# Optimization experiments

Measured on AMD Instinct MI355X. Metric: run time of the kernel, lower is better.

Reference implementation:

```python
import jax, jax.numpy as jnp
import numpy as np
import math

B, T, D = 1, 2048, 2048
H, HD = 16, 128          # n_head, head_dim = D // H
L = 512                  # latent_dims
RD = 64                  # rope_dims
K = 32                   # top-k selected tokens per query
THETA = 10000.0


def rope_tables(rd, t_max):
    freqs = 1.0 / (THETA ** (jnp.arange(0, rd, 2, dtype=jnp.float32) / rd))
    t = jnp.arange(t_max, dtype=jnp.float32)
    ang = jnp.outer(t, freqs)                      # (T, rd/2)
    cos = jnp.concatenate([jnp.cos(ang), jnp.cos(ang)], axis=-1)  # (T, rd)
    sin = jnp.concatenate([jnp.sin(ang), jnp.sin(ang)], axis=-1)
    return cos, sin


def rotate_half(x):
    d = x.shape[-1] // 2
    return jnp.concatenate([-x[..., d:], x[..., :d]], axis=-1)


def apply_rope(x, cos, sin):
    # x: (B, H, T, rd); cos/sin: (T, rd) -> broadcast over B, H
    t = x.shape[2]
    return x * cos[None, None, :t] + rotate_half(x) * sin[None, None, :t]


def setup_inputs() -> dict:
    key = jax.random.key(0)
    ks = jax.random.split(key, 10)
    s = lambda fan_in: 1.0 / math.sqrt(fan_in)
    inp = {
        'x': jax.random.normal(ks[0], (B, T, D), dtype=jnp.float32),
        'Wqd': jax.random.normal(ks[1], (D, L), dtype=jnp.float32) * s(D),
        'Wqu': jax.random.normal(ks[2], (L, D), dtype=jnp.float32) * s(L),
        'Wqr': jax.random.normal(ks[3], (L, H * RD), dtype=jnp.float32) * s(L),
        'Wkvd': jax.random.normal(ks[4], (D, L), dtype=jnp.float32) * s(D),
        'Wku': jax.random.normal(ks[5], (L, D), dtype=jnp.float32) * s(L),
        'Wvu': jax.random.normal(ks[6], (L, D), dtype=jnp.float32) * s(L),
        'Wkr': jax.random.normal(ks[7], (D, RD), dtype=jnp.float32) * s(D),
        'Wo': jax.random.normal(ks[8], (D, D), dtype=jnp.float32) * s(D),
        'topk_idx': jax.random.randint(ks[9], (B, T, K), 0, T, dtype=jnp.int64)
            if jax.config.jax_enable_x64 else
            jax.random.randint(ks[9], (B, T, K), 0, T, dtype=jnp.int32),
    }
    return inp


def reference(x, Wqd, Wqu, Wqr, Wkvd, Wku, Wvu, Wkr, Wo, topk_idx):
    cos, sin = rope_tables(RD, T)

    ql = x @ Wqd                                               # (B,T,L)
    q = (ql @ Wqu).reshape(B, T, H, HD).transpose(0, 2, 1, 3)  # (B,H,T,hd)
    qr = (ql @ Wqr).reshape(B, T, H, RD).transpose(0, 2, 1, 3)
    qr = apply_rope(qr, cos, sin)                              # (B,H,T,rd)

    ckv = x @ Wkvd                                             # (B,T,L)
    k = (ckv @ Wku).reshape(B, T, H, HD).transpose(0, 2, 1, 3) # (B,H,T,hd)
    v = (ckv @ Wvu).reshape(B, T, H, HD).transpose(0, 2, 1, 3)
    kr = apply_rope((x @ Wkr)[:, None], cos, sin)[:, 0]        # (B,T,rd) shared across heads

    # top-k gather sparse attention path
    flat = topk_idx.reshape(B, T * K)                          # (B, T*K)
    k_sel = jax.vmap(lambda a, i: a[:, i])(k, flat).reshape(B, H, T, K, HD)
    v_sel = jax.vmap(lambda a, i: a[:, i])(v, flat).reshape(B, H, T, K, HD)
    kr_sel = jax.vmap(lambda a, i: a[i])(kr, flat).reshape(B, T, K, RD)

    scale = 1.0 / math.sqrt(HD + RD)
    scores = (jnp.einsum('bhtd,bhtkd->bhtk', q, k_sel)
              + jnp.einsum('bhtd,btkd->bhtk', qr, kr_sel)) * scale
    attn = jax.nn.softmax(scores, axis=-1)                     # (B,H,T,K)
    out = jnp.einsum('bhtk,bhtkd->bhtd', attn, v_sel)          # (B,H,T,hd)
    out = out.transpose(0, 2, 1, 3).reshape(B, T, D)
    return out @ Wo
```

## Files before the change

### kernel.cpp

```cpp
#include <hip/hip_runtime.h>
#include <hip/hip_bf16.h>
#include <math.h>

typedef __hip_bfloat16 bf16;
typedef __attribute__((ext_vector_type(4))) float f32x4;
typedef __attribute__((ext_vector_type(8))) short s16x8;

#define T_SEQ 2048
#define DIM   2048
#define NH    16
#define LAT   512
#define RD    64
#define TOPK  32

typedef const __attribute__((address_space(1))) void* gas_ptr;
typedef __attribute__((address_space(3))) void* las_ptr;

struct GGroup {
    const bf16* A; const bf16* BT; bf16* C;
    int K, lda, ldb, ldc;
    int tx, ty, nz;
    long aZ, bZ, cZ;
    int tiles;
    int flags, N, t0;
};
struct GPack { GGroup g[4]; int n; };

template<int MT, int DB>
__global__ __launch_bounds__(256)
void gemm_group(GPack gp)
{
    constexpr int MI = MT / 64;

    int b = blockIdx.x;
    int gi = 0;
    while (gi < gp.n - 1 && b >= gp.g[gi].tiles) { b -= gp.g[gi].tiles; ++gi; }
    const GGroup g = gp.g[gi];

    {
        const int nwg = g.tiles;
        const int xcd = b & 7, idx = b >> 3;
        const int qq = nwg >> 3, rr = nwg & 7;
        b = (xcd < rr ? xcd * (qq + 1) : rr * (qq + 1) + (xcd - rr) * qq) + idx;
    }

    const int per_z = g.tx * g.ty;
    const int z   = b / per_z;
    const int rem = b - z * per_z;
    const int bx  = rem % g.tx;
    const int by  = rem / g.tx;

    const bf16* A  = g.A  + (size_t)z * g.aZ;
    const bf16* BT = g.BT + (size_t)z * g.bZ;
    bf16*       C  = g.C  + (size_t)z * g.cZ;

    __shared__ bf16 aL[(DB + 1) * MT * 64];
    __shared__ bf16 bL[(DB + 1) * 64 * 64];

    const int tid  = threadIdx.x;
    const int wave = tid >> 6;
    const int lane = tid & 63;
    const int quad = lane >> 4;
    const int l16  = lane & 15;

    const int tile_m = by * MT;
    const int tile_n = bx * 64;
    const int wrow = wave * (MT / 4);

    const int lrow = lane >> 3;
    const int lke  = (((lane & 7) ^ lrow) * 8);
    const int sw   = l16 & 7;

    f32x4 acc[MI][4] = {};

    const int nt = g.K >> 6;

    auto stage = [&](int t, int sb) {
        const int k0 = t << 6;
#pragma unroll
        for (int p = 0; p < 2 * MI; ++p) {
            const int R = (wave * 2 * MI + p) * 8;
            const bf16* src = A + (size_t)(tile_m + R + lrow) * g.lda + k0 + lke;
            __builtin_amdgcn_global_load_lds((gas_ptr)src,
                (las_ptr)(aL + sb * MT * 64 + R * 64), 16, 0, 0);
        }
#pragma unroll
        for (int p = 0; p < 2; ++p) {
            const int R = (wave * 2 + p) * 8;
            int brow = tile_n + R + lrow;
            if (g.flags & 2) brow = brow < g.N ? brow : g.N - 1;
            const bf16* src = BT + (size_t)brow * g.ldb + k0 + lke;
            __builtin_amdgcn_global_load_lds((gas_ptr)src,
                (las_ptr)(bL + sb * 4096 + R * 64), 16, 0, 0);
        }
    };

    auto compute = [&](int sb) {
#pragma unroll
        for (int ks = 0; ks < 2; ++ks) {
            s16x8 af[MI], bfr[4];
#pragma unroll
            for (int i = 0; i < MI; ++i)
                af[i] = *(const s16x8*)(&aL[sb * MT * 64 + (wrow + i * 16 + l16) * 64 +
                                            (((ks * 4 + quad) ^ sw) * 8)]);
#pragma unroll
            for (int j = 0; j < 4; ++j)
                bfr[j] = *(const s16x8*)(&bL[sb * 4096 + (j * 16 + l16) * 64 +
                                             (((ks * 4 + quad) ^ sw) * 8)]);

#pragma unroll
            for (int i = 0; i < MI; ++i)
#pragma unroll
                for (int j = 0; j < 4; ++j)
                    acc[i][j] = __builtin_amdgcn_mfma_f32_16x16x32_bf16(
                        af[i], bfr[j], acc[i][j], 0, 0, 0);
        }
    };

    if (DB) {
        stage(0, 0);
        asm volatile("s_waitcnt vmcnt(0)" ::: "memory");
        __builtin_amdgcn_s_barrier();
        int cur = 0;
        for (int t = 0; t < nt; ++t) {
            if (t + 1 < nt) stage(t + 1, cur ^ 1);
            compute(cur);
            asm volatile("s_waitcnt vmcnt(0)" ::: "memory");
            __builtin_amdgcn_s_barrier();
            cur ^= 1;
        }
    } else {
        for (int t = 0; t < nt; ++t) {
            stage(t, 0);
            __syncthreads();
            compute(0);
            __syncthreads();
        }
    }

    if (g.flags & 1) {
#pragma unroll
        for (int jp = 0; jp < 2; ++jp) {
            const int colL = tile_n + jp * 16 + l16;
            if ((g.flags & 2) && colL >= g.N) continue;
            const float fr = powf(10000.f, -(float)(jp * 16 + l16) / 32.f);
#pragma unroll
            for (int i = 0; i < MI; ++i) {
#pragma unroll
                for (int r = 0; r < 4; ++r) {
                    const int row = tile_m + wrow + i * 16 + quad * 4 + r;
                    float sv, cv;
                    sincosf((float)(g.t0 + row) * fr, &sv, &cv);
                    const float x0 = acc[i][jp][r];
                    const float x1 = acc[i][jp + 2][r];
                    C[(size_t)row * g.ldc + colL]      = __float2bfloat16(x0 * cv - x1 * sv);
                    C[(size_t)row * g.ldc + colL + 32] = __float2bfloat16(x1 * cv + x0 * sv);
                }
            }
        }
    } else if (g.flags & 4) {
        float* Cf = (float*)C;
#pragma unroll
        for (int j = 0; j < 4; ++j) {
            const int col = tile_n + j * 16 + l16;
#pragma unroll
            for (int i = 0; i < MI; ++i)
#pragma unroll
                for (int r = 0; r < 4; ++r) {
                    const int row = tile_m + wrow + i * 16 + quad * 4 + r;
                    Cf[(size_t)row * g.ldc + col] = acc[i][j][r];
                }
        }
    } else {
#pragma unroll
        for (int j = 0; j < 4; ++j) {
            const int col = tile_n + j * 16 + l16;
            if ((g.flags & 2) && col >= g.N) continue;
#pragma unroll
            for (int i = 0; i < MI; ++i)
#pragma unroll
                for (int r = 0; r < 4; ++r) {
                    const int row = tile_m + wrow + i * 16 + quad * 4 + r;
                    C[(size_t)row * g.ldc + col] = __float2bfloat16(acc[i][j][r]);
                }
        }
    }
}

template<int DB>
__global__ __launch_bounds__(256)
void gemm128(GPack gp)
{
    int b = blockIdx.x;
    int gi = 0;
    while (gi < gp.n - 1 && b >= gp.g[gi].tiles) { b -= gp.g[gi].tiles; ++gi; }
    const GGroup g = gp.g[gi];

    {
        const int nwg = g.tiles;
        const int xcd = b & 7, idx = b >> 3;
        const int qq = nwg >> 3, rr = nwg & 7;
        b = (xcd < rr ? xcd * (qq + 1) : rr * (qq + 1) + (xcd - rr) * qq) + idx;
    }

    const int per_z = g.tx * g.ty;
    const int z   = b / per_z;
    const int rem = b - z * per_z;
    const int bx  = rem % g.tx;
    const int by  = rem / g.tx;

    const bf16* A  = g.A  + (size_t)z * g.aZ;
    const bf16* BT = g.BT + (size_t)z * g.bZ;
    bf16*       C  = g.C  + (size_t)z * g.cZ;

    __shared__ bf16 aL[(DB + 1) * 128 * 64];
    __shared__ bf16 bL[(DB + 1) * 128 * 64];

    const int tid  = threadIdx.x;
    const int wave = tid >> 6;
    const int lane = tid & 63;
    const int quad = lane >> 4;
    const int l16  = lane & 15;

    const int tile_m = by * 128;
    const int tile_n = bx * 128;
    const int wm = (wave >> 1) * 64;
    const int wn = (wave & 1) * 64;

    const int lrow = lane >> 3;
    const int lke  = (((lane & 7) ^ lrow) * 8);
    const int sw   = l16 & 7;

    f32x4 acc[4][4] = {};

    const int nt = g.K >> 6;

    auto stage = [&](int t, int sb) {
        const int k0 = t << 6;
#pragma unroll
        for (int p = 0; p < 4; ++p) {
            const int R = (wave * 4 + p) * 8;
            const bf16* srcA = A + (size_t)(tile_m + R + lrow) * g.lda + k0 + lke;
            __builtin_amdgcn_global_load_lds((gas_ptr)srcA,
                (las_ptr)(aL + sb * 8192 + R * 64), 16, 0, 0);
            int brow = tile_n + R + lrow;
            if (g.flags & 2) brow = brow < g.N ? brow : g.N - 1;
            const bf16* srcB = BT + (size_t)brow * g.ldb + k0 + lke;
            __builtin_amdgcn_global_load_lds((gas_ptr)srcB,
                (las_ptr)(bL + sb * 8192 + R * 64), 16, 0, 0);
        }
    };

    auto compute = [&](int sb) {
#pragma unroll
        for (int ks = 0; ks < 2; ++ks) {
            const int seg = ((ks * 4 + quad) ^ sw) * 8;
            s16x8 af[4], bf_[4];
#pragma unroll
            for (int i = 0; i < 4; ++i)
                af[i] = *(const s16x8*)(&aL[sb * 8192 + (wm + i * 16 + l16) * 64 + seg]);
#pragma unroll
            for (int j = 0; j < 4; ++j)
                bf_[j] = *(const s16x8*)(&bL[sb * 8192 + (wn + j * 16 + l16) * 64 + seg]);

#pragma unroll
            for (int i = 0; i < 4; ++i)
#pragma unroll
                for (int j = 0; j < 4; ++j)
                    acc[i][j] = __builtin_amdgcn_mfma_f32_16x16x32_bf16(
                        af[i], bf_[j], acc[i][j], 0, 0, 0);
        }
    };

    if (DB) {
        stage(0, 0);
        asm volatile("s_waitcnt vmcnt(0)" ::: "memory");
        __builtin_amdgcn_s_barrier();
        int cur = 0;
        for (int t = 0; t < nt; ++t) {
            if (t + 1 < nt) stage(t + 1, cur ^ 1);
            compute(cur);
            asm volatile("s_waitcnt vmcnt(0)" ::: "memory");
            __builtin_amdgcn_s_barrier();
            cur ^= 1;
        }
    } else {
        for (int t = 0; t < nt; ++t) {
            stage(t, 0);
            __syncthreads();
            compute(0);
            __syncthreads();
        }
    }

    if (g.flags & 1) {
#pragma unroll
        for (int jp = 0; jp < 2; ++jp) {
            const int colL = tile_n + wn + jp * 16 + l16;
            if ((g.flags & 2) && colL >= g.N) continue;
            const float fr = powf(10000.f, -(float)(jp * 16 + l16) / 32.f);
#pragma unroll
            for (int i = 0; i < 4; ++i) {
#pragma unroll
                for (int r = 0; r < 4; ++r) {
                    const int row = tile_m + wm + i * 16 + quad * 4 + r;
                    float sv, cv;
                    sincosf((float)(g.t0 + row) * fr, &sv, &cv);
                    const float x0 = acc[i][jp][r];
                    const float x1 = acc[i][jp + 2][r];
                    C[(size_t)row * g.ldc + colL]      = __float2bfloat16(x0 * cv - x1 * sv);
                    C[(size_t)row * g.ldc + colL + 32] = __float2bfloat16(x1 * cv + x0 * sv);
                }
            }
        }
    } else if (g.flags & 4) {
        float* Cf = (float*)C;
#pragma unroll
        for (int j = 0; j < 4; ++j) {
            const int col = tile_n + wn + j * 16 + l16;
#pragma unroll
            for (int i = 0; i < 4; ++i)
#pragma unroll
                for (int r = 0; r < 4; ++r) {
                    const int row = tile_m + wm + i * 16 + quad * 4 + r;
                    Cf[(size_t)row * g.ldc + col] = acc[i][j][r];
                }
        }
    } else {
#pragma unroll
        for (int j = 0; j < 4; ++j) {
            const int col = tile_n + wn + j * 16 + l16;
            if ((g.flags & 2) && col >= g.N) continue;
#pragma unroll
            for (int i = 0; i < 4; ++i)
#pragma unroll
                for (int r = 0; r < 4; ++r) {
                    const int row = tile_m + wm + i * 16 + quad * 4 + r;
                    C[(size_t)row * g.ldc + col] = __float2bfloat16(acc[i][j][r]);
                }
        }
    }
}

struct TDesc { const float* src; bf16* dst; int R; int C; int tiles; int ctiles; };
struct TPack { TDesc d[8]; int n; };

__global__ __launch_bounds__(256)
void transpose_batch(TPack p)
{
    int b = blockIdx.x;
    int mi = 0;
    while (mi < p.n - 1 && b >= p.d[mi].tiles) { b -= p.d[mi].tiles; ++mi; }
    const TDesc d = p.d[mi];
    const int tr = b / d.ctiles, tc = b % d.ctiles;
    const int r0 = tr * 32, c0 = tc * 32;

    __shared__ float lds[32][33];
    const int tx = threadIdx.x & 31, ty = threadIdx.x >> 5;
#pragma unroll
    for (int i = 0; i < 4; ++i)
        lds[ty * 4 + i][tx] = d.src[(size_t)(r0 + ty * 4 + i) * d.C + c0 + tx];
    __syncthreads();
#pragma unroll
    for (int i = 0; i < 4; ++i)
        d.dst[(size_t)(c0 + ty * 4 + i) * d.R + r0 + tx] =
            __float2bfloat16(lds[tx][ty * 4 + i]);
}

__global__ __launch_bounds__(256)
void convert2(const float* s0, bf16* d0, int n0,
              const float* s1, bf16* d1, int n1)
{
    int i = blockIdx.x * blockDim.x + threadIdx.x;
    const float* s; bf16* d;
    if (i < n0) { s = s0; d = d0; }
    else if (i < n0 + n1) { i -= n0; s = s1; d = d1; }
    else return;
    const float4 a = *(const float4*)(s + (size_t)i * 8);
    const float4 b = *(const float4*)(s + (size_t)i * 8 + 4);
    bf16 t[8];
    t[0] = __float2bfloat16(a.x); t[1] = __float2bfloat16(a.y);
    t[2] = __float2bfloat16(a.z); t[3] = __float2bfloat16(a.w);
    t[4] = __float2bfloat16(b.x); t[5] = __float2bfloat16(b.y);
    t[6] = __float2bfloat16(b.z); t[7] = __float2bfloat16(b.w);
    *(uint4*)(d + (size_t)i * 8) = *(uint4*)t;
}

__global__ __launch_bounds__(256)
void reduce2(float* out, const float* a, const float* b, int n4)
{
    int i = blockIdx.x * blockDim.x + threadIdx.x;
    if (i < n4) {
        float4 x = ((const float4*)a)[i];
        const float4 y = ((const float4*)b)[i];
        x.x += y.x; x.y += y.y; x.z += y.z; x.w += y.w;
        ((float4*)out)[i] = x;
    }
}

__global__ __launch_bounds__(256)
void attn_mla(const bf16* __restrict__ qt,
              const bf16* __restrict__ qr,
              const bf16* __restrict__ xw,
              const bf16* __restrict__ kr,
              const int*  __restrict__ topk,
              bf16* __restrict__ U,
              int t0)
{
    __shared__ short ckv_s[32 * 520];
    __shared__ short kr_s[32 * 72];
    __shared__ short qr_s[16 * 72];
    __shared__ short P_s[4][16 * 40];
    __shared__ float red[4][64][4];
    __shared__ int   idx_s[32];

    const int tl   = blockIdx.x;
    const int tg   = t0 + tl;
    const int tid  = threadIdx.x;
    const int wv   = tid >> 6;
    const int lane = tid & 63;
    const int quad = lane >> 4;
    const int l16  = lane & 15;

    if (tid < 32) {
        int j = topk[(size_t)tg * TOPK + tid];
        idx_s[tid] = (j < 0 || j >= T_SEQ) ? 0 : j;
    }
    __syncthreads();

#pragma unroll
    for (int i = 0; i < 8; ++i) {
        const int row = wv * 8 + i;
        const int j = idx_s[row];
        __builtin_amdgcn_global_load_lds(
            (gas_ptr)(xw + (size_t)j * 1024 + 512 + lane * 8),
            (las_ptr)(ckv_s + row * 520), 16, 0, 0);
    }
    {
        const int row = tid >> 3, seg = tid & 7;
        const int j = idx_s[row];
        *(uint4*)(kr_s + row * 72 + seg * 8) =
            *(const uint4*)(kr + (size_t)j * RD + seg * 8);
    }
    if (tid < 128) {
        const int head = tid >> 3, seg = tid & 7;
        *(uint4*)(qr_s + head * 72 + seg * 8) =
            *(const uint4*)(qr + (size_t)tl * 1024 + head * 64 + seg * 8);
    }
    __syncthreads();

    const bf16* qrow = qt + (size_t)tl * 8192 + l16 * 512;
    f32x4 sc[2] = {};
#pragma unroll
    for (int kk = 0; kk < 4; ++kk) {
        const int ks = wv * 4 + kk;
        s16x8 a  = *(const s16x8*)(qrow + ks * 32 + quad * 8);
        s16x8 b0 = *(const s16x8*)(ckv_s + l16 * 520 + ks * 32 + quad * 8);
        s16x8 b1 = *(const s16x8*)(ckv_s + (16 + l16) * 520 + ks * 32 + quad * 8);
        sc[0] = __builtin_amdgcn_mfma_f32_16x16x32_bf16(a, b0, sc[0], 0, 0, 0);
        sc[1] = __builtin_amdgcn_mfma_f32_16x16x32_bf16(a, b1, sc[1], 0, 0, 0);
    }
    if (wv < 2) {
        const int ks = wv;
        s16x8 a  = *(const s16x8*)(qr_s + l16 * 72 + ks * 32 + quad * 8);
        s16x8 b0 = *(const s16x8*)(kr_s + l16 * 72 + ks * 32 + quad * 8);
        s16x8 b1 = *(const s16x8*)(kr_s + (16 + l16) * 72 + ks * 32 + quad * 8);
        sc[0] = __builtin_amdgcn_mfma_f32_16x16x32_bf16(a, b0, sc[0], 0, 0, 0);
        sc[1] = __builtin_amdgcn_mfma_f32_16x16x32_bf16(a, b1, sc[1], 0, 0, 0);
    }

    *(f32x4*)red[wv][lane] = sc[0];
    __syncthreads();
    sc[0] = *(const f32x4*)red[0][lane] + *(const f32x4*)red[1][lane] +
            *(const f32x4*)red[2][lane] + *(const f32x4*)red[3][lane];
    __syncthreads();
    *(f32x4*)red[wv][lane] = sc[1];
    __syncthreads();
    sc[1] = *(const f32x4*)red[0][lane] + *(const f32x4*)red[1][lane] +
            *(const f32x4*)red[2][lane] + *(const f32x4*)red[3][lane];

    const float scale = 0.0721687836487032f;
    float inv[4];
    short* pw = P_s[wv];
#pragma unroll
    for (int r = 0; r < 4; ++r) {
        float s0 = sc[0][r] * scale, s1 = sc[1][r] * scale;
        float mx = fmaxf(s0, s1);
#pragma unroll
        for (int off = 1; off < 16; off <<= 1) mx = fmaxf(mx, __shfl_xor(mx, off));
        float p0 = __expf(s0 - mx), p1 = __expf(s1 - mx);
        float l = p0 + p1;
#pragma unroll
        for (int off = 1; off < 16; off <<= 1) l += __shfl_xor(l, off);
        inv[r] = 1.f / l;
        pw[(quad * 4 + r) * 40 + l16]      = __builtin_bit_cast(short, __float2bfloat16(p0));
        pw[(quad * 4 + r) * 40 + 16 + l16] = __builtin_bit_cast(short, __float2bfloat16(p1));
    }

    s16x8 ap = *(const s16x8*)(pw + l16 * 40 + quad * 8);
#pragma unroll
    for (int tt = 0; tt < 8; ++tt) {
        const int n0 = wv * 128 + tt * 16;
        s16x8 b;
#pragma unroll
        for (int j = 0; j < 8; ++j)
            b[j] = ckv_s[(quad * 8 + j) * 520 + n0 + l16];
        f32x4 u = {};
        u = __builtin_amdgcn_mfma_f32_16x16x32_bf16(ap, b, u, 0, 0, 0);
#pragma unroll
        for (int r = 0; r < 4; ++r)
            U[(size_t)tl * 8192 + (quad * 4 + r) * 512 + n0 + l16] =
                __float2bfloat16(u[r] * inv[r]);
    }
}

extern "C" void kernel_launch(void* const* d_in, const int* in_sizes, int n_in,
                              void* d_out, int out_size, void* d_ws, size_t ws_size,
                              hipStream_t stream)
{
    const float* x    = (const float*)d_in[0];
    const float* Wqd  = (const float*)d_in[1];
    const float* Wqu  = (const float*)d_in[2];
    const float* Wqr  = (const float*)d_in[3];
    const float* Wkvd = (const float*)d_in[4];
    const float* Wku  = (const float*)d_in[5];
    const float* Wvu  = (const float*)d_in[6];
    const float* Wkr  = (const float*)d_in[7];
    const float* Wo   = (const float*)d_in[8];
    const int*   topk = (const int*)d_in[9];
    float* out = (float*)d_out;

    const size_t KB = 1024;
    char* ws = (char*)d_ws;
    const bool flat = ws_size >= (size_t)128000 * KB;
    const int  TCH  = flat ? 2048 : 512;
    const int  NCH  = T_SEQ / TCH;

    size_t oXB, oWxT, oWkrT, oWquT, oWkub, oWqrT, oWvuT, oQ, oXW, oKR,
           oQR, oO, oWoT, oQT, oU;
    if (flat) {
        oXB = 0;       oWxT = 8192;   oWkrT = 12288; oWquT = 12544;
        oWkub = 14592; oWqrT = 16640; oWvuT = 17664; oQ = 19712;
        oXW = 27904;   oKR = 32000;   oQR = 32256;   oO = 36352;
        oWoT = 44544;  oQT = 52736;   oU = 85504;
    } else {
        oXW = 0;       oKR = 4096;    oWquT = 4352;  oWkub = 6400;
        oWqrT = 8448;  oWvuT = 9472;  oO = 11520;    oXB = 19712;
        oWxT = 27904;  oWkrT = 32000; oQ = 19712;    oQT = 21760;
        oQR = 29952;   oU = 30976;    oWoT = 21760;
    }
    bf16* xb   = (bf16*)(ws + oXB * KB);
    bf16* WxT  = (bf16*)(ws + oWxT * KB);
    bf16* WkrT = (bf16*)(ws + oWkrT * KB);
    bf16* WquT = (bf16*)(ws + oWquT * KB);
    bf16* Wkub = (bf16*)(ws + oWkub * KB);
    bf16* WqrT = (bf16*)(ws + oWqrT * KB);
    bf16* WvuT = (bf16*)(ws + oWvuT * KB);
    bf16* qB   = (bf16*)(ws + oQ * KB);
    bf16* xw   = (bf16*)(ws + oXW * KB);
    bf16* kr   = (bf16*)(ws + oKR * KB);
    bf16* qrC  = (bf16*)(ws + oQR * KB);
    bf16* o    = (bf16*)(ws + oO * KB);
    bf16* WoT  = (bf16*)(ws + oWoT * KB);
    bf16* qtC  = (bf16*)(ws + oQT * KB);
    bf16* uC   = (bf16*)(ws + oU * KB);

    dim3 blk(256);

    {
        int n0 = T_SEQ * DIM / 8, n1 = LAT * DIM / 8;
        convert2<<<(n0 + n1 + 255) / 256, blk, 0, stream>>>(x, xb, n0, Wku, Wkub, n1);
        TPack p;
        p.d[0] = { Wqd,  WxT,                   DIM, LAT,  (DIM/32)*(LAT/32),  LAT/32 };
        p.d[1] = { Wkvd, WxT + (size_t)LAT*DIM, DIM, LAT,  (DIM/32)*(LAT/32),  LAT/32 };
        p.d[2] = { Wkr,  WkrT,                  DIM, RD,   (DIM/32)*(RD/32),   RD/32  };
        p.d[3] = { Wqr,  WqrT,                  LAT, 1024, (LAT/32)*(1024/32), 1024/32 };
        p.d[4] = { Wvu,  WvuT,                  LAT, DIM,  (LAT/32)*(DIM/32),  DIM/32 };
        p.d[5] = { Wqu,  WquT,                  LAT, DIM,  (LAT/32)*(DIM/32),  DIM/32 };
        p.n = 6;
        int tot = 0;
        for (int i = 0; i < p.n; ++i) tot += p.d[i].tiles;
        if (flat) {
            p.d[6] = { Wo, WoT, DIM, DIM, (DIM/32)*(DIM/32), DIM/32 };
            p.n = 7; tot += p.d[6].tiles;
        }
        transpose_batch<<<tot, blk, 0, stream>>>(p);
    }

    {
        GPack gp;
        gp.g[0] = { xb, WxT,  xw, DIM, DIM, DIM, 1024, 1024/64, T_SEQ/64, 1,
                    0, 0, 0, (1024/64)*(T_SEQ/64), 0, 1024, 0 };
        gp.g[1] = { xb, WkrT, kr, DIM, DIM, DIM, RD,   1,       T_SEQ/64, 1,
                    0, 0, 0, T_SEQ/64, 1 , RD, 0 };
        gp.n = 2;
        gemm_group<64, 1><<<gp.g[0].tiles + gp.g[1].tiles, blk, 0, stream>>>(gp);
    }

    for (int c = 0; c < NCH; ++c) {
        const int t0 = c * TCH;
        bf16* q  = flat ? qB  + (size_t)t0 * 2048 : qB;
        bf16* qt = flat ? qtC + (size_t)t0 * 8192 : qtC;
        bf16* qr = flat ? qrC + (size_t)t0 * 1024 : qrC;
        bf16* U  = flat ? uC  + (size_t)t0 * 8192 : uC;
        const bf16* xwc = xw + (size_t)t0 * 1024;

        {
            GPack gp;
            gp.g[0] = { xwc, WquT, q,  LAT, 1024, LAT, 2048, 2048/64, TCH/128, 1,
                        0, 0, 0, (2048/64)*(TCH/128), 0, 2048, 0 };
            gp.g[1] = { xwc, WqrT, qr, LAT, 1024, LAT, 1024, 1024/64, TCH/128, 1,
                        0, 0, 0, (1024/64)*(TCH/128), 1 , 1024, t0 };
            gp.n = 2;
            gemm_group<128, 1><<<gp.g[0].tiles + gp.g[1].tiles, blk, 0, stream>>>(gp);
        }
        {
            GPack gp;
            gp.g[0] = { q, Wkub, qt, 128, 2048, 2048, 8192, 512/128, TCH/128, NH,
                        128, 128, 512, (512/128)*(TCH/128)*NH, 0, 512, 0 };
            gp.n = 1;
            gemm128<0><<<gp.g[0].tiles, blk, 0, stream>>>(gp);
        }
        attn_mla<<<TCH, blk, 0, stream>>>(qt, qr, xw, kr, topk, U, t0);
        {
            GPack gp;
            gp.g[0] = { U, WvuT, o + (size_t)t0 * DIM, LAT, 8192, LAT, DIM,
                        2, TCH/128, NH, 512, (long)128*LAT, 128,
                        2*(TCH/128)*NH, 0, 128, 0 };
            gp.n = 1;
            gemm_group<128, 1><<<gp.g[0].tiles, blk, 0, stream>>>(gp);
        }
    }

    if (!flat) {
        TPack p;
        p.d[0] = { Wo, WoT, DIM, DIM, (DIM/32)*(DIM/32), DIM/32 };
        p.n = 1;
        transpose_batch<<<p.d[0].tiles, blk, 0, stream>>>(p);
        GPack gp;
        gp.g[0] = { o, WoT, (bf16*)out, DIM, DIM, DIM, DIM,
                    DIM/64, T_SEQ/128, 1, 0, 0, 0,
                    (DIM/64)*(T_SEQ/128), 4 , DIM, 0 };
        gp.n = 1;
        gemm_group<128, 0><<<gp.g[0].tiles, blk, 0, stream>>>(gp);
    } else {
        float* part = (float*)(ws + oQT * KB);
        GPack gp;
        gp.g[0] = { o, WoT, (bf16*)part, 1024, DIM, DIM, DIM,
                    DIM/128, T_SEQ/128, 2, 1024, 1024,
                    (long)T_SEQ * DIM * 2 ,
                    (DIM/128)*(T_SEQ/128)*2, 4 , DIM, 0 };
        gp.n = 1;
        gemm128<1><<<gp.g[0].tiles, blk, 0, stream>>>(gp);
        reduce2<<<(T_SEQ * DIM / 4 + 255) / 256, blk, 0, stream>>>(
            out, part, part + (size_t)T_SEQ * DIM, T_SEQ * DIM / 4);
    }
}
```

Baseline: 236.8 us.

## Merge convert and transpose launches; XOR-swizzle gathered ckv rows in LDS

The separate fp32-to-bf16 convert kernel and the weight-transpose batch kernel become one launch that dispatches on block index, which removes a kernel launch and the gap between them. In the attention kernel, the gathered ckv rows are stored in LDS with an XOR swizzle on 16-byte segments. The score-MFMA reads and the transposed P·V reads use matching swizzled addresses, which is meant to reduce LDS bank conflicts. The swizzle indexing adds some address arithmetic and has to stay consistent between the writes and both read paths.

```diff
diff --git a/kernel.cpp b/kernel.cpp
--- a/kernel.cpp
+++ b/kernel.cpp
@@ -386,6 +386,50 @@
     *(uint4*)(d + (size_t)i * 8) = *(uint4*)t;
 }
 
+struct APack {
+    const float* s0; bf16* d0; int n0;
+    const float* s1; bf16* d1; int n1;
+    int cblocks;
+    TPack tp;
+};
+
+__global__ __launch_bounds__(256)
+void phaseA(APack p)
+{
+    __shared__ float lds[32][33];
+    if ((int)blockIdx.x < p.cblocks) {
+        int i = blockIdx.x * blockDim.x + threadIdx.x;
+        const float* s; bf16* d;
+        if (i < p.n0) { s = p.s0; d = p.d0; }
+        else if (i < p.n0 + p.n1) { i -= p.n0; s = p.s1; d = p.d1; }
+        else return;
+        const float4 a = *(const float4*)(s + (size_t)i * 8);
+        const float4 b = *(const float4*)(s + (size_t)i * 8 + 4);
+        bf16 t[8];
+        t[0] = __float2bfloat16(a.x); t[1] = __float2bfloat16(a.y);
+        t[2] = __float2bfloat16(a.z); t[3] = __float2bfloat16(a.w);
+        t[4] = __float2bfloat16(b.x); t[5] = __float2bfloat16(b.y);
+        t[6] = __float2bfloat16(b.z); t[7] = __float2bfloat16(b.w);
+        *(uint4*)(d + (size_t)i * 8) = *(uint4*)t;
+        return;
+    }
+    int b = blockIdx.x - p.cblocks;
+    int mi = 0;
+    while (mi < p.tp.n - 1 && b >= p.tp.d[mi].tiles) { b -= p.tp.d[mi].tiles; ++mi; }
+    const TDesc d = p.tp.d[mi];
+    const int tr = b / d.ctiles, tc = b % d.ctiles;
+    const int r0 = tr * 32, c0 = tc * 32;
+    const int tx = threadIdx.x & 31, ty = threadIdx.x >> 5;
+#pragma unroll
+    for (int i = 0; i < 4; ++i)
+        lds[ty * 4 + i][tx] = d.src[(size_t)(r0 + ty * 4 + i) * d.C + c0 + tx];
+    __syncthreads();
+#pragma unroll
+    for (int i = 0; i < 4; ++i)
+        d.dst[(size_t)(c0 + ty * 4 + i) * d.R + r0 + tx] =
+            __float2bfloat16(lds[tx][ty * 4 + i]);
+}
+
 __global__ __launch_bounds__(256)
 void reduce2(float* out, const float* a, const float* b, int n4)
 {
@@ -433,7 +477,7 @@
         const int row = wv * 8 + i;
         const int j = idx_s[row];
         __builtin_amdgcn_global_load_lds(
-            (gas_ptr)(xw + (size_t)j * 1024 + 512 + lane * 8),
+            (gas_ptr)(xw + (size_t)j * 1024 + 512 + ((lane ^ wv) * 8)),
             (las_ptr)(ckv_s + row * 520), 16, 0, 0);
     }
     {
@@ -450,13 +494,16 @@
     __syncthreads();
 
     const bf16* qrow = qt + (size_t)tl * 8192 + l16 * 512;
+    const int h0 = l16 >> 3;
     f32x4 sc[2] = {};
 #pragma unroll
     for (int kk = 0; kk < 4; ++kk) {
         const int ks = wv * 4 + kk;
         s16x8 a  = *(const s16x8*)(qrow + ks * 32 + quad * 8);
-        s16x8 b0 = *(const s16x8*)(ckv_s + l16 * 520 + ks * 32 + quad * 8);
-        s16x8 b1 = *(const s16x8*)(ckv_s + (16 + l16) * 520 + ks * 32 + quad * 8);
+        s16x8 b0 = *(const s16x8*)(ckv_s + l16 * 520 +
+                                   (((ks * 4 + quad) ^ h0) * 8));
+        s16x8 b1 = *(const s16x8*)(ckv_s + (16 + l16) * 520 +
+                                   (((ks * 4 + quad) ^ (2 + h0)) * 8));
         sc[0] = __builtin_amdgcn_mfma_f32_16x16x32_bf16(a, b0, sc[0], 0, 0, 0);
         sc[1] = __builtin_amdgcn_mfma_f32_16x16x32_bf16(a, b1, sc[1], 0, 0, 0);
     }
@@ -501,10 +548,11 @@
 #pragma unroll
     for (int tt = 0; tt < 8; ++tt) {
         const int n0 = wv * 128 + tt * 16;
+        const int cs = (n0 >> 3) + h0;
         s16x8 b;
 #pragma unroll
         for (int j = 0; j < 8; ++j)
-            b[j] = ckv_s[(quad * 8 + j) * 520 + n0 + l16];
+            b[j] = ckv_s[(quad * 8 + j) * 520 + ((cs ^ quad) << 3) + (l16 & 7)];
         f32x4 u = {};
         u = __builtin_amdgcn_mfma_f32_16x16x32_bf16(ap, b, u, 0, 0, 0);
 #pragma unroll
@@ -569,8 +617,11 @@
 
     {
         int n0 = T_SEQ * DIM / 8, n1 = LAT * DIM / 8;
-        convert2<<<(n0 + n1 + 255) / 256, blk, 0, stream>>>(x, xb, n0, Wku, Wkub, n1);
-        TPack p;
+        APack ap;
+        ap.s0 = x;   ap.d0 = xb;   ap.n0 = n0;
+        ap.s1 = Wku; ap.d1 = Wkub; ap.n1 = n1;
+        ap.cblocks = (n0 + n1 + 255) / 256;
+        TPack& p = ap.tp;
         p.d[0] = { Wqd,  WxT,                   DIM, LAT,  (DIM/32)*(LAT/32),  LAT/32 };
         p.d[1] = { Wkvd, WxT + (size_t)LAT*DIM, DIM, LAT,  (DIM/32)*(LAT/32),  LAT/32 };
         p.d[2] = { Wkr,  WkrT,                  DIM, RD,   (DIM/32)*(RD/32),   RD/32  };
@@ -584,7 +635,7 @@
             p.d[6] = { Wo, WoT, DIM, DIM, (DIM/32)*(DIM/32), DIM/32 };
             p.n = 7; tot += p.d[6].tiles;
         }
-        transpose_batch<<<tot, blk, 0, stream>>>(p);
+        phaseA<<<ap.cblocks + tot, blk, 0, stream>>>(ap);
     }
 
     {
```

Result: no change. 234.6 us (-0.9%).
